# Kernel tuning notes

Hardware: AMD Instinct MI355X
Metric: run time of the kernel (lower is better)

The kernel has to match this reference:

```python
import jax, jax.numpy as jnp
import numpy as np

HEADS = 8
D_MODEL = 512
D_K = D_MODEL // HEADS


def setup_inputs() -> dict:
    key = jax.random.key(0)
    k1, k2, k3, k4 = jax.random.split(key, 4)
    N, S = 4, 2048
    queries = jax.random.normal(k1, (N, S, D_MODEL), dtype=jnp.float32)
    keys = jax.random.normal(k2, (N, S, D_MODEL), dtype=jnp.float32)
    values = jax.random.normal(k3, (N, S, D_MODEL), dtype=jnp.float32)
    W_out = jax.random.normal(k4, (D_MODEL, D_MODEL), dtype=jnp.float32) * (1.0 / np.sqrt(D_MODEL))
    b_out = jnp.zeros((D_MODEL,), dtype=jnp.float32)
    return {"queries": queries, "keys": keys, "values": values, "W_out": W_out, "b_out": b_out}


def reference(queries, keys, values, W_out, b_out):
    N, Q, _ = queries.shape
    K = keys.shape[1]
    # NOTE: the original module defines q/k/v Linear layers but never applies
    # them in forward; inputs are reshaped directly into heads.
    q = queries.reshape(N, Q, HEADS, D_K)
    k = keys.reshape(N, K, HEADS, D_K)
    v = values.reshape(N, K, HEADS, D_K)
    # energy: [N, H, Q, K] -- full score matrix materialized, as in source
    energy = jnp.einsum('nqhd,nkhd->nhqk', q, k)
    # Quirk preserved: scale by sqrt(d_model), not sqrt(d_k)
    attn_w = jax.nn.softmax(energy / np.sqrt(D_MODEL), axis=3)
    attention = jnp.einsum('nhql,nlhd->nqhd', attn_w, v).reshape(N, Q, D_MODEL)
    # fc_output: torch Linear computes x @ W.T + b
    out = attention @ W_out.T + b_out
    return out
```

## Files before the change

kernel.cpp:

```cpp
#include <hip/hip_runtime.h>
#include <hip/hip_bf16.h>
#include <cstdint>
#include <cstddef>

#define S_LEN 2048
#define DM 512
#define DK 64

typedef __attribute__((ext_vector_type(4))) float f32x4;
typedef __attribute__((ext_vector_type(8))) short short8;
typedef __attribute__((ext_vector_type(8))) _Float16 f16x8;

__device__ __forceinline__ unsigned short f2bf(float f) {
  union { float f; uint32_t u; } c; c.f = f;
  uint32_t u = c.u;
  u += 0x7FFF + ((u >> 16) & 1);
  return (unsigned short)(u >> 16);
}

__device__ __forceinline__ unsigned short f2h(float f) {
  union { _Float16 h; unsigned short u; } c; c.h = (_Float16)f; return c.u;
}

__device__ __forceinline__ unsigned int pkbf(float a, float b) {
  union { __hip_bfloat162 h; unsigned int u; } c;
  c.h = __float22bfloat162_rn(make_float2(a, b));
  return c.u;
}

__device__ __forceinline__ unsigned int pkh(float a, float b) {
  auto pk = __builtin_amdgcn_cvt_pkrtz(a, b);
  union { decltype(pk) h; unsigned int u; } c;
  c.h = pk;
  return c.u;
}

__device__ __forceinline__ short8 ldq8(const float* p, float s) {
  float4 a = *reinterpret_cast<const float4*>(p);
  float4 b = *reinterpret_cast<const float4*>(p + 4);
  union { short8 v; unsigned int u[4]; } r;
  r.u[0] = pkbf(a.x * s, a.y * s);
  r.u[1] = pkbf(a.z * s, a.w * s);
  r.u[2] = pkbf(b.x * s, b.y * s);
  r.u[3] = pkbf(b.z * s, b.w * s);
  return r.v;
}

__device__ __forceinline__ void gl2lds16(const unsigned short* g, unsigned short* l) {
  __builtin_amdgcn_global_load_lds(
      (const __attribute__((address_space(1))) unsigned int*)g,
      (__attribute__((address_space(3))) unsigned int*)l, 16, 0, 0);
}

#define SWAP32(a, b) asm volatile("v_permlane32_swap_b32 %0, %1" : "+v"(a), "+v"(b))
#define SWAP16(a, b) asm volatile("v_permlane16_swap_b32 %0, %1" : "+v"(a), "+v"(b))

__global__ __launch_bounds__(256) void prep_kernel(const float* __restrict__ K,
                                                   const float* __restrict__ V,
                                                   const float* __restrict__ W,
                                                   unsigned short* __restrict__ Kb,
                                                   unsigned short* __restrict__ Vt,
                                                   unsigned short* __restrict__ Wb) {
  __shared__ unsigned short tile[64][66];
  const int bid = blockIdx.x;
  const int t = threadIdx.x;
  if (bid < 4096) {
    int i = (bid * 256 + t) * 4;
    float4 v = *reinterpret_cast<const float4*>(K + i);
    ushort4 o;
    o.x = f2bf(v.x); o.y = f2bf(v.y); o.z = f2bf(v.z); o.w = f2bf(v.w);
    *reinterpret_cast<ushort4*>(Kb + i) = o;
  } else if (bid < 4352) {
    int i = ((bid - 4096) * 256 + t) * 4;
    float4 v = *reinterpret_cast<const float4*>(W + i);
    ushort4 o;
    o.x = f2bf(v.x); o.y = f2bf(v.y); o.z = f2bf(v.z); o.w = f2bf(v.w);
    *reinterpret_cast<ushort4*>(Wb + i) = o;
  } else {
    const int r = bid - 4352;
    const int lt = r & 31;
    const int nh = r >> 5;
    const int n = nh >> 3, h = nh & 7;
    #pragma unroll
    for (int it = 0; it < 16; ++it) {
      int e = it * 256 + t;
      int l = e >> 6, d = e & 63;
      float v = V[((size_t)(n * S_LEN + lt * 64 + l)) * DM + h * DK + d];
      tile[l][d] = f2h(v);
    }
    __syncthreads();
    #pragma unroll
    for (int it = 0; it < 16; ++it) {
      int e = it * 256 + t;
      int d = e >> 6, l = e & 63;
      Vt[((size_t)(nh * DK + d)) * S_LEN + lt * 64 + l] = tile[l][d];
    }
  }
}

__global__ __launch_bounds__(256, 4) void attn_kernel(const float* __restrict__ Qf,
                                                      const unsigned short* __restrict__ Kb,
                                                      const unsigned short* __restrict__ Vt,
                                                      unsigned short* __restrict__ Ab) {
  __shared__ __align__(16) unsigned short KT[2][64 * 64];
  __shared__ __align__(16) unsigned short VT[2][64 * 64];
  __shared__ float lsL[2][2][16];

  const int dlin = blockIdx.x + 32 * blockIdx.y;
  const int xcd = dlin & 7;
  const int mm = dlin >> 3;
  const int nh = xcd * 4 + (mm & 3);
  const int qtb = mm >> 2;
  const int n = nh >> 3, h = nh & 7;
  const int wave = threadIdx.x >> 6;
  const int lane = threadIdx.x & 63;
  const int c = lane & 15;
  const int g = lane >> 4;
  const int qw = wave >> 1;
  const int kw = wave & 1;
  const int c7 = c & 7;

  const int qbase = qtb * 64 + qw * 32;
  const float C2 = 0.063758716f;

  short8 qfrag[2][2];
  #pragma unroll
  for (int qt = 0; qt < 2; ++qt)
    #pragma unroll
    for (int dkc = 0; dkc < 2; ++dkc)
      qfrag[qt][dkc] = ldq8(
          Qf + ((size_t)(n * S_LEN + qbase + qt * 16 + c)) * DM + h * DK + dkc * 32 + g * 8, C2);

  f32x4 oacc[2][4];
  #pragma unroll
  for (int qt = 0; qt < 2; ++qt)
    #pragma unroll
    for (int dt = 0; dt < 4; ++dt) oacc[qt][dt] = (f32x4){0.f, 0.f, 0.f, 0.f};
  float lsum[2] = {0.f, 0.f};

  const int srow = lane >> 3;
  const int csrc = (lane & 7) ^ srow;
  const unsigned short* ksrc = Kb + ((size_t)(n * S_LEN + srow)) * DM + h * DK + csrc * 8;
  const unsigned short* vsrc = Vt + ((size_t)(nh * DK + srow)) * S_LEN + csrc * 8;
  const int kr0 = wave * 16;

#define STAGE(B_, L0_) do {                                                        \
    _Pragma("unroll")                                                              \
    for (int u = 0; u < 2; ++u)                                                    \
      gl2lds16(ksrc + (size_t)((L0_) + kr0 + u * 8) * DM, &KT[B_][(kr0 + u * 8) * 64]); \
    _Pragma("unroll")                                                              \
    for (int u = 0; u < 2; ++u)                                                    \
      gl2lds16(vsrc + (size_t)(kr0 + u * 8) * S_LEN + (L0_), &VT[B_][(kr0 + u * 8) * 64]); \
  } while (0)

#define COMPUTE(B_) do {                                                           \
    short8 kf[2][2];                                                               \
    _Pragma("unroll")                                                              \
    for (int ks = 0; ks < 2; ++ks)                                                 \
      _Pragma("unroll")                                                            \
      for (int dkc = 0; dkc < 2; ++dkc)                                            \
        kf[ks][dkc] = *reinterpret_cast<const short8*>(                            \
            &KT[B_][(kw * 32 + ks * 16 + c) * 64 + (((dkc * 4 + g) ^ c7) << 3)]);  \
    f32x4 s[2][2];                                                                 \
    _Pragma("unroll")                                                              \
    for (int qt = 0; qt < 2; ++qt)                                                 \
      _Pragma("unroll")                                                            \
      for (int ks = 0; ks < 2; ++ks) s[qt][ks] = (f32x4){0.f, 0.f, 0.f, 0.f};      \
    _Pragma("unroll")                                                              \
    for (int dkc = 0; dkc < 2; ++dkc)                                              \
      _Pragma("unroll")                                                            \
      for (int ks = 0; ks < 2; ++ks)                                               \
        _Pragma("unroll")                                                          \
        for (int qt = 0; qt < 2; ++qt)                                             \
          s[qt][ks] = __builtin_amdgcn_mfma_f32_16x16x32_bf16(                     \
              kf[ks][dkc], qfrag[qt][dkc], s[qt][ks], 0, 0, 0);                    \
    union { f16x8 v; unsigned int u[4]; } pf[2];                                   \
    _Pragma("unroll")                                                              \
    for (int qt = 0; qt < 2; ++qt) {                                               \
      float pa0 = __builtin_amdgcn_exp2f(s[qt][0][0]);                             \
      float pa1 = __builtin_amdgcn_exp2f(s[qt][0][1]);                             \
      float pa2 = __builtin_amdgcn_exp2f(s[qt][0][2]);                             \
      float pa3 = __builtin_amdgcn_exp2f(s[qt][0][3]);                             \
      float pb0 = __builtin_amdgcn_exp2f(s[qt][1][0]);                             \
      float pb1 = __builtin_amdgcn_exp2f(s[qt][1][1]);                             \
      float pb2 = __builtin_amdgcn_exp2f(s[qt][1][2]);                             \
      float pb3 = __builtin_amdgcn_exp2f(s[qt][1][3]);                             \
      lsum[qt] += ((pa0 + pa1) + (pa2 + pa3)) + ((pb0 + pb1) + (pb2 + pb3));       \
      unsigned int pA = pkh(pa0, pa1);                                             \
      unsigned int pB = pkh(pa2, pa3);                                             \
      unsigned int pC = pkh(pb0, pb1);                                             \
      unsigned int pD = pkh(pb2, pb3);                                             \
      SWAP32(pA, pC); SWAP32(pB, pD);                                              \
      SWAP16(pA, pC); SWAP16(pB, pD);                                              \
      pf[qt].u[0] = pA; pf[qt].u[1] = pB; pf[qt].u[2] = pC; pf[qt].u[3] = pD;      \
    }                                                                              \
    _Pragma("unroll")                                                              \
    for (int dt = 0; dt < 4; ++dt) {                                               \
      const f16x8 vf = *reinterpret_cast<const f16x8*>(                            \
          &VT[B_][(dt * 16 + c) * 64 + (((kw * 4 + g) ^ c7) << 3)]);               \
      _Pragma("unroll")                                                            \
      for (int qt = 0; qt < 2; ++qt)                                               \
        oacc[qt][dt] = __builtin_amdgcn_mfma_f32_16x16x32_f16(                     \
            vf, pf[qt].v, oacc[qt][dt], 0, 0, 0);                                  \
    }                                                                              \
  } while (0)

  STAGE(0, 0);
  asm volatile("s_waitcnt vmcnt(0)" ::: "memory");
  __syncthreads();

  for (int l0 = 0; l0 < S_LEN; l0 += 64) {
    const int cur = (l0 >> 6) & 1;
    if (l0 + 64 < S_LEN) STAGE(cur ^ 1, l0 + 64);
    COMPUTE(cur);
    __syncthreads();
  }
#undef STAGE
#undef COMPUTE

  #pragma unroll
  for (int qt = 0; qt < 2; ++qt) {
    lsum[qt] += __shfl_xor(lsum[qt], 16);
    lsum[qt] += __shfl_xor(lsum[qt], 32);
  }

  float* red = reinterpret_cast<float*>(&KT[0][0]);
  if (kw == 1) {
    #pragma unroll
    for (int qt = 0; qt < 2; ++qt)
      #pragma unroll
      for (int dt = 0; dt < 4; ++dt)
        *reinterpret_cast<f32x4*>(red + (((qw * 2 + qt) * 4 + dt) << 8) + lane * 4) = oacc[qt][dt];
    if (lane < 16) { lsL[qw][0][lane] = lsum[0]; lsL[qw][1][lane] = lsum[1]; }
  }
  __syncthreads();
  if (kw == 0) {
    #pragma unroll
    for (int qt = 0; qt < 2; ++qt) {
      #pragma unroll
      for (int dt = 0; dt < 4; ++dt)
        oacc[qt][dt] += *reinterpret_cast<const f32x4*>(
            red + (((qw * 2 + qt) * 4 + dt) << 8) + lane * 4);
      const float rl = 1.f / (lsum[qt] + lsL[qw][qt][c]);
      unsigned short* ab = Ab + ((size_t)(n * S_LEN + qbase + qt * 16 + c)) * DM + h * DK;
      #pragma unroll
      for (int dt = 0; dt < 4; ++dt) {
        uint2 w;
        w.x = pkbf(oacc[qt][dt][0] * rl, oacc[qt][dt][1] * rl);
        w.y = pkbf(oacc[qt][dt][2] * rl, oacc[qt][dt][3] * rl);
        *reinterpret_cast<uint2*>(ab + dt * 16 + g * 4) = w;
      }
    }
  }
}

__global__ __launch_bounds__(256, 2) void proj_kernel(const unsigned short* __restrict__ Ab,
                                                      const unsigned short* __restrict__ Wb,
                                                      const float* __restrict__ bias,
                                                      float* __restrict__ out) {
  __shared__ __align__(16) unsigned short At[2][128 * 64];
  __shared__ __align__(16) unsigned short Wt[2][64 * 64];

  const int m0 = blockIdx.x * 128;
  const int o0 = blockIdx.y * 64;
  const int wave = threadIdx.x >> 6;
  const int lane = threadIdx.x & 63;
  const int lr = lane & 15;
  const int lg = lane >> 4;
  const int r7 = lr & 7;
  const int wm = (wave >> 1) * 64;
  const int wn = (wave & 1) * 32;

  const int srow = lane >> 3;
  const int csrc = (lane & 7) ^ srow;
  const unsigned short* asrc = Ab + ((size_t)(m0 + wave * 32 + srow)) * DM + csrc * 8;
  const unsigned short* wsrc = Wb + ((size_t)(o0 + wave * 16 + srow)) * DM + csrc * 8;

  float bv[2];
  #pragma unroll
  for (int nf = 0; nf < 2; ++nf) bv[nf] = bias[o0 + wn + nf * 16 + lr];

  f32x4 acc[4][2];
  #pragma unroll
  for (int mf = 0; mf < 4; ++mf)
    #pragma unroll
    for (int nf = 0; nf < 2; ++nf) acc[mf][nf] = (f32x4){0.f, 0.f, 0.f, 0.f};

#define PSTAGE(B_, KB_) do {                                                       \
    _Pragma("unroll")                                                              \
    for (int u = 0; u < 4; ++u)                                                    \
      gl2lds16(asrc + (size_t)(u * 8) * DM + (KB_), &At[B_][(wave * 32 + u * 8) * 64]); \
    _Pragma("unroll")                                                              \
    for (int u = 0; u < 2; ++u)                                                    \
      gl2lds16(wsrc + (size_t)(u * 8) * DM + (KB_), &Wt[B_][(wave * 16 + u * 8) * 64]); \
  } while (0)

#define PCOMPUTE(B_) do {                                                          \
    _Pragma("unroll")                                                              \
    for (int kc = 0; kc < 2; ++kc) {                                               \
      const int sw = ((kc * 4 + lg) ^ r7) << 3;                                    \
      short8 af[4], wf[2];                                                         \
      _Pragma("unroll")                                                            \
      for (int mf = 0; mf < 4; ++mf)                                               \
        af[mf] = *reinterpret_cast<const short8*>(&At[B_][(wm + mf * 16 + lr) * 64 + sw]); \
      _Pragma("unroll")                                                            \
      for (int nf = 0; nf < 2; ++nf)                                               \
        wf[nf] = *reinterpret_cast<const short8*>(&Wt[B_][(wn + nf * 16 + lr) * 64 + sw]); \
      _Pragma("unroll")                                                            \
      for (int mf = 0; mf < 4; ++mf)                                               \
        _Pragma("unroll")                                                          \
        for (int nf = 0; nf < 2; ++nf)                                             \
          acc[mf][nf] = __builtin_amdgcn_mfma_f32_16x16x32_bf16(af[mf], wf[nf], acc[mf][nf], 0, 0, 0); \
    }                                                                              \
  } while (0)

  PSTAGE(0, 0);
  asm volatile("s_waitcnt vmcnt(0)" ::: "memory");
  __syncthreads();

  for (int kb = 0; kb < DM; kb += 64) {
    const int cur = (kb >> 6) & 1;
    if (kb + 64 < DM) PSTAGE(cur ^ 1, kb + 64);
    PCOMPUTE(cur);
    __syncthreads();
  }
#undef PSTAGE
#undef PCOMPUTE

  #pragma unroll
  for (int mf = 0; mf < 4; ++mf) {
    #pragma unroll
    for (int j = 0; j < 4; ++j) {
      float* op = out + (size_t)(m0 + wm + mf * 16 + lg * 4 + j) * DM + o0 + wn + lr;
      #pragma unroll
      for (int nf = 0; nf < 2; ++nf)
        op[nf * 16] = acc[mf][nf][j] + bv[nf];
    }
  }
}

extern "C" void kernel_launch(void* const* d_in, const int* in_sizes, int n_in,
                              void* d_out, int out_size, void* d_ws, size_t ws_size,
                              hipStream_t stream) {
  const float* Q = (const float*)d_in[0];
  const float* K = (const float*)d_in[1];
  const float* V = (const float*)d_in[2];
  const float* W = (const float*)d_in[3];
  const float* b = (const float*)d_in[4];
  float* out = (float*)d_out;

  char* ws = (char*)d_ws;
  unsigned short* Kb = (unsigned short*)(ws);
  unsigned short* Vt = (unsigned short*)(ws + 8388608);
  unsigned short* Ab = (unsigned short*)(ws + 16777216);
  unsigned short* Wb = (unsigned short*)(ws + 25165824);

  prep_kernel<<<5376, 256, 0, stream>>>(K, V, W, Kb, Vt, Wb);
  attn_kernel<<<dim3(32, 32), 256, 0, stream>>>(Q, Kb, Vt, Ab);
  proj_kernel<<<dim3(64, 8), 256, 0, stream>>>(Ab, Wb, b, out);
}
```

Before: 73.60 us.

## Double KV tile per iteration and split K/V loading across wave pairs

Each main-loop iteration of the attention kernel now stages 128 keys instead of 64. Each wave processes two 32-key sub-chunks, which halves the number of block barriers and loop iterations. Staging is reassigned so waves 0-1 load K and waves 2-3 load V, with eight 16-byte loads each. The shared-memory footprint doubles and launch bounds drop from 4 to 2 blocks per CU, so the change trades occupancy and latency hiding for less synchronization overhead.

Result: slower. 76.20 us (+3.5%).

```diff
diff --git a/kernel.cpp b/kernel.cpp
--- a/kernel.cpp
+++ b/kernel.cpp
@@ -98,12 +98,12 @@
   }
 }
 
-__global__ __launch_bounds__(256, 4) void attn_kernel(const float* __restrict__ Qf,
+__global__ __launch_bounds__(256, 2) void attn_kernel(const float* __restrict__ Qf,
                                                       const unsigned short* __restrict__ Kb,
                                                       const unsigned short* __restrict__ Vt,
                                                       unsigned short* __restrict__ Ab) {
-  __shared__ __align__(16) unsigned short KT[2][64 * 64];
-  __shared__ __align__(16) unsigned short VT[2][64 * 64];
+  __shared__ __align__(16) unsigned short KT[2][2][64 * 64];
+  __shared__ __align__(16) unsigned short VT[2][2][64 * 64];
   __shared__ float lsL[2][2][16];
 
   const int dlin = blockIdx.x + 32 * blockIdx.y;
@@ -140,27 +140,34 @@
 
   const int srow = lane >> 3;
   const int csrc = (lane & 7) ^ srow;
-  const unsigned short* ksrc = Kb + ((size_t)(n * S_LEN + srow)) * DM + h * DK + csrc * 8;
-  const unsigned short* vsrc = Vt + ((size_t)(nh * DK + srow)) * S_LEN + csrc * 8;
-  const int kr0 = wave * 16;
+  const int sub = wave & 1;
+  const bool isK = (wave < 2);
+  const unsigned short* sbase = isK
+      ? Kb + ((size_t)(n * S_LEN + sub * 64 + srow)) * DM + h * DK + csrc * 8
+      : Vt + ((size_t)(nh * DK + srow)) * S_LEN + sub * 64 + csrc * 8;
+  unsigned short* dbase[2] = { isK ? &KT[0][sub][0] : &VT[0][sub][0],
+                               isK ? &KT[1][sub][0] : &VT[1][sub][0] };
 
 #define STAGE(B_, L0_) do {                                                        \
-    _Pragma("unroll")                                                              \
-    for (int u = 0; u < 2; ++u)                                                    \
-      gl2lds16(ksrc + (size_t)((L0_) + kr0 + u * 8) * DM, &KT[B_][(kr0 + u * 8) * 64]); \
-    _Pragma("unroll")                                                              \
-    for (int u = 0; u < 2; ++u)                                                    \
-      gl2lds16(vsrc + (size_t)(kr0 + u * 8) * S_LEN + (L0_), &VT[B_][(kr0 + u * 8) * 64]); \
+    if (isK) {                                                                     \
+      _Pragma("unroll")                                                            \
+      for (int u = 0; u < 8; ++u)                                                  \
+        gl2lds16(sbase + (size_t)((L0_) + u * 8) * DM, dbase[B_] + (u * 8) * 64);  \
+    } else {                                                                       \
+      _Pragma("unroll")                                                            \
+      for (int u = 0; u < 8; ++u)                                                  \
+        gl2lds16(sbase + (size_t)(u * 8) * S_LEN + (L0_), dbase[B_] + (u * 8) * 64); \
+    }                                                                              \
   } while (0)
 
-#define COMPUTE(B_) do {                                                           \
+#define COMPUTE32(B_, KS2_) do {                                                   \
     short8 kf[2][2];                                                               \
     _Pragma("unroll")                                                              \
     for (int ks = 0; ks < 2; ++ks)                                                 \
       _Pragma("unroll")                                                            \
       for (int dkc = 0; dkc < 2; ++dkc)                                            \
         kf[ks][dkc] = *reinterpret_cast<const short8*>(                            \
-            &KT[B_][(kw * 32 + ks * 16 + c) * 64 + (((dkc * 4 + g) ^ c7) << 3)]);  \
+            &KT[B_][kw][((KS2_) * 32 + ks * 16 + c) * 64 + (((dkc * 4 + g) ^ c7) << 3)]); \
     f32x4 s[2][2];                                                                 \
     _Pragma("unroll")                                                              \
     for (int qt = 0; qt < 2; ++qt)                                                 \
@@ -197,7 +204,7 @@
     _Pragma("unroll")                                                              \
     for (int dt = 0; dt < 4; ++dt) {                                               \
       const f16x8 vf = *reinterpret_cast<const f16x8*>(                            \
-          &VT[B_][(dt * 16 + c) * 64 + (((kw * 4 + g) ^ c7) << 3)]);               \
+          &VT[B_][kw][(dt * 16 + c) * 64 + ((((KS2_) * 4 + g) ^ c7) << 3)]);       \
       _Pragma("unroll")                                                            \
       for (int qt = 0; qt < 2; ++qt)                                               \
         oacc[qt][dt] = __builtin_amdgcn_mfma_f32_16x16x32_f16(                     \
@@ -209,14 +216,15 @@
   asm volatile("s_waitcnt vmcnt(0)" ::: "memory");
   __syncthreads();
 
-  for (int l0 = 0; l0 < S_LEN; l0 += 64) {
-    const int cur = (l0 >> 6) & 1;
-    if (l0 + 64 < S_LEN) STAGE(cur ^ 1, l0 + 64);
-    COMPUTE(cur);
+  for (int l0 = 0; l0 < S_LEN; l0 += 128) {
+    const int cur = (l0 >> 7) & 1;
+    if (l0 + 128 < S_LEN) STAGE(cur ^ 1, l0 + 128);
+    COMPUTE32(cur, 0);
+    COMPUTE32(cur, 1);
     __syncthreads();
   }
 #undef STAGE
-#undef COMPUTE
+#undef COMPUTE32
 
   #pragma unroll
   for (int qt = 0; qt < 2; ++qt) {
@@ -224,7 +232,7 @@
     lsum[qt] += __shfl_xor(lsum[qt], 32);
   }
 
-  float* red = reinterpret_cast<float*>(&KT[0][0]);
+  float* red = reinterpret_cast<float*>(&KT[0][0][0]);
   if (kw == 1) {
     #pragma unroll
     for (int qt = 0; qt < 2; ++qt)
```
